# Kernel optimization log

Measured on AMD Instinct MI355X. Metric: run time of the kernel, lower is better.

Reference implementation:

```python
import jax, jax.numpy as jnp
import numpy as np

THRESH = 0.5
TAU = 0.5
GAMMA = 1.0
BETA = 0.9
A = 0.5
B = 0.5


def zif_spike(v):
    # ZIF surrogate: forward is hard threshold (v > 0).
    return (v > 0).astype(v.dtype)


def setup_inputs() -> dict:
    key = jax.random.key(0)
    x = jax.random.normal(key, (64, 8192, 100), dtype=jnp.float32)
    return {"x": x}


def reference(x):
    # x: [B, N, T]; scan over time with (mem, w) state kept per element.
    xt = jnp.moveaxis(x, 2, 0)  # [T, B, N]
    init_mem = jnp.zeros(xt.shape[1:], dtype=x.dtype)
    init_w = jnp.zeros(xt.shape[1:], dtype=x.dtype)

    def step(carry, x_t):
        mem, w = carry
        mem = mem * TAU + x_t - w
        spike = zif_spike(mem - THRESH)
        w = BETA * w + (1.0 - BETA) * (A * mem + B * spike)
        mem = mem - spike * THRESH  # soft reset
        return (mem, w), spike

    _, spikes = jax.lax.scan(step, (init_mem, init_w), xt)  # [T, B, N]
    return jnp.moveaxis(spikes, 0, 2)  # [B, N, T]
```

## Files before the change

### kernel.cpp

```cpp
#include <hip/hip_runtime.h>

#define T_STEPS 100
#define CHUNKS  25
#define TPB     64
#define ELEMS   64

typedef const __attribute__((address_space(1))) unsigned int g_u32;
typedef __attribute__((address_space(3))) unsigned int l_u32;

__global__ __launch_bounds__(TPB) void lif_kernel(const float* __restrict__ x,
                                                  float* __restrict__ out) {
#pragma clang fp contract(off)
    __shared__ float4 tile[ELEMS * CHUNKS];

    const int lane = threadIdx.x;
    const size_t tile4 = (size_t)blockIdx.x * (ELEMS * CHUNKS);
    const float4* __restrict__ xb = (const float4*)x + tile4;
    float4* __restrict__ ob = (float4*)out + tile4;

#pragma unroll
    for (int k = 0; k < CHUNKS; ++k) {
        __builtin_amdgcn_global_load_lds(
            (g_u32*)(xb + k * TPB + lane),
            (l_u32*)&tile[k * TPB],
            16, 0, 0);
    }
    __syncthreads();

    {
        float mem = 0.0f;
        float w = 0.0f;
#pragma unroll
        for (int c = 0; c < CHUNKS; ++c) {
            float4 xv4 = tile[lane * CHUNKS + c];
            float xv[4] = {xv4.x, xv4.y, xv4.z, xv4.w};
            float sv[4];
#pragma unroll
            for (int j = 0; j < 4; ++j) {
                mem = (mem * 0.5f + xv[j]) - w;
                float spike = (mem - 0.5f) > 0.0f ? 1.0f : 0.0f;
                w = 0.9f * w + 0.1f * (0.5f * mem + 0.5f * spike);
                mem = mem - spike * 0.5f;
                sv[j] = spike;
            }
            float4 s4;
            s4.x = sv[0]; s4.y = sv[1]; s4.z = sv[2]; s4.w = sv[3];
            tile[lane * CHUNKS + c] = s4;
        }
    }
    __syncthreads();

#pragma unroll
    for (int k = 0; k < CHUNKS; ++k) {
        float4 s = tile[k * TPB + lane];
        ob[k * TPB + lane] = s;
    }
}

extern "C" void kernel_launch(void* const* d_in, const int* in_sizes, int n_in,
                              void* d_out, int out_size, void* d_ws, size_t ws_size,
                              hipStream_t stream) {
    const float* x = (const float*)d_in[0];
    float* out = (float*)d_out;
    int n_elem = in_sizes[0] / T_STEPS;
    int grid = n_elem / ELEMS;

    lif_kernel<<<grid, TPB, 0, stream>>>(x, out);
}
```

Measured before the change: 346.6 us.

## Use persistent blocks with prefetch of next tile and bitpacked spike transpose

Switches to a persistent grid of 1536 single-wave blocks that loop over tiles. Each block loads its tile from LDS into registers, then issues the async global-to-LDS prefetch of the next tile so the load overlaps compute and stores. Spikes are packed into bitmasks and transposed across lanes with ds_bpermute, removing the LDS writeback and both __syncthreads. The cost is heavier register use (25 float4 held per lane), manual waitcnt handling that relies on single-wave blocks, and extra ALU work to unpack the bits.

```diff
diff --git a/kernel.cpp b/kernel.cpp
--- a/kernel.cpp
+++ b/kernel.cpp
@@ -4,56 +4,96 @@
 #define CHUNKS  25
 #define TPB     64
 #define ELEMS   64
+#define PGRID   1536
 
 typedef const __attribute__((address_space(1))) unsigned int g_u32;
 typedef __attribute__((address_space(3))) unsigned int l_u32;
 
 __global__ __launch_bounds__(TPB) void lif_kernel(const float* __restrict__ x,
-                                                  float* __restrict__ out) {
+                                                  float* __restrict__ out,
+                                                  int nt) {
 #pragma clang fp contract(off)
     __shared__ float4 tile[ELEMS * CHUNKS];
 
     const int lane = threadIdx.x;
-    const size_t tile4 = (size_t)blockIdx.x * (ELEMS * CHUNKS);
-    const float4* __restrict__ xb = (const float4*)x + tile4;
-    float4* __restrict__ ob = (float4*)out + tile4;
-
-#pragma unroll
-    for (int k = 0; k < CHUNKS; ++k) {
-        __builtin_amdgcn_global_load_lds(
-            (g_u32*)(xb + k * TPB + lane),
-            (l_u32*)&tile[k * TPB],
-            16, 0, 0);
-    }
-    __syncthreads();
+    int ti = blockIdx.x;
+    if (ti >= nt) return;
 
     {
-        float mem = 0.0f;
-        float w = 0.0f;
+        const float4* __restrict__ xb = (const float4*)x + (size_t)ti * (ELEMS * CHUNKS);
+#pragma unroll
+        for (int k = 0; k < CHUNKS; ++k) {
+            __builtin_amdgcn_global_load_lds(
+                (g_u32*)(xb + k * TPB + lane), (l_u32*)&tile[k * TPB], 16, 0, 0);
+        }
+    }
+    asm volatile("s_waitcnt vmcnt(0)" ::: "memory");
+    __builtin_amdgcn_sched_barrier(0);
+
+    while (true) {
+        float4 xv[CHUNKS];
+#pragma unroll
+        for (int c = 0; c < CHUNKS; ++c) xv[c] = tile[lane * CHUNKS + c];
+        asm volatile("s_waitcnt lgkmcnt(0)" ::: "memory");
+        __builtin_amdgcn_sched_barrier(0);
+
+        const int nxt = ti + PGRID;
+        if (nxt < nt) {
+            const float4* __restrict__ xb = (const float4*)x + (size_t)nxt * (ELEMS * CHUNKS);
+#pragma unroll
+            for (int k = 0; k < CHUNKS; ++k) {
+                __builtin_amdgcn_global_load_lds(
+                    (g_u32*)(xb + k * TPB + lane), (l_u32*)&tile[k * TPB], 16, 0, 0);
+            }
+        }
+
+        unsigned b0 = 0, b1 = 0, b2 = 0, b3 = 0;
+        float mem = 0.0f, w = 0.0f;
 #pragma unroll
         for (int c = 0; c < CHUNKS; ++c) {
-            float4 xv4 = tile[lane * CHUNKS + c];
-            float xv[4] = {xv4.x, xv4.y, xv4.z, xv4.w};
-            float sv[4];
+            float xs[4] = {xv[c].x, xv[c].y, xv[c].z, xv[c].w};
 #pragma unroll
             for (int j = 0; j < 4; ++j) {
-                mem = (mem * 0.5f + xv[j]) - w;
-                float spike = (mem - 0.5f) > 0.0f ? 1.0f : 0.0f;
+                mem = (mem * 0.5f + xs[j]) - w;
+                const bool fire = (mem - 0.5f) > 0.0f;
+                const float spike = fire ? 1.0f : 0.0f;
                 w = 0.9f * w + 0.1f * (0.5f * mem + 0.5f * spike);
                 mem = mem - spike * 0.5f;
-                sv[j] = spike;
+                const int t = c * 4 + j;
+                const unsigned bit = fire ? 1u : 0u;
+                if (t < 32)      b0 |= bit << t;
+                else if (t < 64) b1 |= bit << (t - 32);
+                else if (t < 96) b2 |= bit << (t - 64);
+                else             b3 |= bit << (t - 96);
             }
-            float4 s4;
-            s4.x = sv[0]; s4.y = sv[1]; s4.z = sv[2]; s4.w = sv[3];
-            tile[lane * CHUNKS + c] = s4;
         }
-    }
-    __syncthreads();
 
+        float4* __restrict__ ob = (float4*)out + (size_t)ti * (ELEMS * CHUNKS);
 #pragma unroll
-    for (int k = 0; k < CHUNKS; ++k) {
-        float4 s = tile[k * TPB + lane];
-        ob[k * TPB + lane] = s;
+        for (int k = 0; k < CHUNKS; ++k) {
+            const int f = k * TPB + lane;
+            const int e = f / 25;
+            const int c = f - e * 25;
+            const int a = e << 2;
+            const unsigned w0 = (unsigned)__builtin_amdgcn_ds_bpermute(a, (int)b0);
+            const unsigned w1 = (unsigned)__builtin_amdgcn_ds_bpermute(a, (int)b1);
+            const unsigned w2 = (unsigned)__builtin_amdgcn_ds_bpermute(a, (int)b2);
+            const unsigned w3 = (unsigned)__builtin_amdgcn_ds_bpermute(a, (int)b3);
+            const unsigned word = (c < 16) ? ((c < 8) ? w0 : w1)
+                                           : ((c < 24) ? w2 : w3);
+            const int sh = (c & 7) * 4;
+            float4 s;
+            s.x = ((word >> (sh + 0)) & 1u) ? 1.0f : 0.0f;
+            s.y = ((word >> (sh + 1)) & 1u) ? 1.0f : 0.0f;
+            s.z = ((word >> (sh + 2)) & 1u) ? 1.0f : 0.0f;
+            s.w = ((word >> (sh + 3)) & 1u) ? 1.0f : 0.0f;
+            ob[f] = s;
+        }
+
+        ti = nxt;
+        if (ti >= nt) break;
+        asm volatile("s_waitcnt vmcnt(25)" ::: "memory");
+        __builtin_amdgcn_sched_barrier(0);
     }
 }
 
@@ -63,7 +103,8 @@
     const float* x = (const float*)d_in[0];
     float* out = (float*)d_out;
     int n_elem = in_sizes[0] / T_STEPS;
-    int grid = n_elem / ELEMS;
+    int nt = n_elem / ELEMS;
+    int grid = nt < PGRID ? nt : PGRID;
 
-    lif_kernel<<<grid, TPB, 0, stream>>>(x, out);
+    lif_kernel<<<grid, TPB, 0, stream>>>(x, out, nt);
 }
```

Result: slower. 361.8 us (+4.4%).
